# Kernel tuning notes

Measured on AMD Instinct MI355X. Metric: run time of the kernel, lower is better.

## Reference

```python
import jax, jax.numpy as jnp
import numpy as np

B, S, H, R, F, E, K = 4, 2048, 1024, 256, 4096, 8, 2


def setup_inputs() -> dict:
    key = jax.random.key(0)
    k = jax.random.split(key, 7)
    s = 0.02
    return {
        "x": jax.random.normal(k[0], (B, S, H), dtype=jnp.float32),
        "router_w": jax.random.normal(k[1], (H, E), dtype=jnp.float32) * s,
        "router_b": jnp.zeros((E,), dtype=jnp.float32),
        "w1": jax.random.normal(k[2], (E, H, R), dtype=jnp.float32) * s,  # expert Linear(hidden->rank), no bias
        "w2": jax.random.normal(k[3], (E, R, F), dtype=jnp.float32) * s,  # expert Linear(rank->ffn), no bias
        "lin2_w": jax.random.normal(k[4], (F, H), dtype=jnp.float32) * s,
        "lin2_b": jnp.zeros((H,), dtype=jnp.float32),
    }


def reference(x, router_w, router_b, w1, w2, lin2_w, lin2_b):
    # Router: softmax over experts, top-k selection (mask), weight by softmax prob
    logits = jnp.einsum("bsh,he->bse", x, router_w) + router_b
    routing_weights = jax.nn.softmax(logits, axis=-1)            # [B,S,E]
    _, topk_idx = jax.lax.top_k(routing_weights, K)              # [B,S,K]
    mask = jnp.sum(jax.nn.one_hot(topk_idx, E, dtype=x.dtype), axis=-2)  # [B,S,E] in {0,1}
    mw = routing_weights * mask                                  # mask * weight per expert

    # Dense per-expert low-rank FFN (original computes all experts, masks after).
    # Fold mask*weight into the rank-space activations to avoid a [B,S,E,F] tensor.
    t = jnp.einsum("bsh,ehr->bser", x, w1)                       # [B,S,E,R]
    t = t * mw[..., None]
    mixed = jnp.einsum("bser,erf->bsf", t, w2)                   # [B,S,F]

    h = jax.nn.gelu(mixed, approximate=False)                    # torch nn.GELU is erf-based
    out = jnp.einsum("bsf,fh->bsh", h, lin2_w) + lin2_b
    # dropout is identity in eval mode
    return out
```

## Files before the change

### kernel.cpp

```cpp
#include <hip/hip_runtime.h>
#include <math.h>


using short8  = __attribute__((ext_vector_type(8))) short;
using floatx4 = __attribute__((ext_vector_type(4))) float;
typedef unsigned short bf16_t;

#define TOK   8192
#define HDIM  1024
#define RDIM  256
#define FDIM  4096
#define NEXP  8
#define MAXTILES 128
#define MAXSLOTS 16384

__device__ __forceinline__ bf16_t f2bf(float f) {
  union { float f; unsigned u; } a; a.f = f;
  unsigned u = a.u;
  return (bf16_t)((u + 0x7FFFu + ((u >> 16) & 1u)) >> 16);
}

__device__ __forceinline__ float gelu_erf(float v) {
  return 0.5f * v * (1.0f + erff(v * 0.70710678118654752f));
}

__device__ __forceinline__ void gload16(const void* g, void* l) {
  __builtin_amdgcn_global_load_lds(
      (const __attribute__((address_space(1))) void*)g,
      (__attribute__((address_space(3))) void*)l, 16, 0, 0);
}


__global__ void tcvt(const float* __restrict__ in, bf16_t* __restrict__ out,
                     int cols, size_t inSlice, size_t ldo,
                     int outRowStep, int outColStep) {
  __shared__ float tile[32][33];
  const int z  = blockIdx.z;
  const float* src = in + (size_t)z * inSlice;
  const int c0 = blockIdx.x * 32;
  const int r0 = blockIdx.y * 32;
  const int tx = threadIdx.x;
  const int ty = threadIdx.y;
#pragma unroll
  for (int i = 0; i < 32; i += 8)
    tile[ty + i][tx] = src[(size_t)(r0 + ty + i) * cols + (c0 + tx)];
  __syncthreads();
#pragma unroll
  for (int i = 0; i < 32; i += 8) {
    float v = tile[tx][ty + i];
    out[((size_t)(c0 + ty + i) + (size_t)z * outRowStep) * ldo +
        (size_t)z * outColStep + (r0 + tx)] = f2bf(v);
  }
}


__global__ void zero_ctrl(int* ctrl) {
  ctrl[blockIdx.x * 256 + threadIdx.x] = 0;
}

__global__ void router_kernel(const float* __restrict__ x,
                              const float* __restrict__ rw,
                              const float* __restrict__ rb,
                              int* __restrict__ ctrl,
                              int* __restrict__ gid_tok,
                              float2* __restrict__ tokscale,
                              bf16_t* __restrict__ xb) {
  const int token = blockIdx.x * 4 + (threadIdx.x >> 6);
  const int lane  = threadIdx.x & 63;
  const float* xr = x + (size_t)token * HDIM;
  bf16_t* xbr = xb + (size_t)token * HDIM;

  double acc[NEXP];
#pragma unroll
  for (int e = 0; e < NEXP; e++) acc[e] = 0.0;
  for (int h = lane; h < HDIM; h += 64) {
    const float xf = xr[h];
    xbr[h] = f2bf(xf);
    const double xv = (double)xf;
    const float* wr = rw + (size_t)h * NEXP;
#pragma unroll
    for (int e = 0; e < NEXP; e++) acc[e] += xv * (double)wr[e];
  }
#pragma unroll
  for (int off = 32; off > 0; off >>= 1) {
#pragma unroll
    for (int e = 0; e < NEXP; e++) acc[e] += __shfl_xor(acc[e], off, 64);
  }
  double lg[NEXP];
#pragma unroll
  for (int e = 0; e < NEXP; e++) lg[e] = acc[e] + (double)rb[e];

  double mx = lg[0];
#pragma unroll
  for (int e = 1; e < NEXP; e++) mx = fmax(mx, lg[e]);
  double p[NEXP]; double den = 0.0;
#pragma unroll
  for (int e = 0; e < NEXP; e++) { p[e] = exp(lg[e] - mx); den += p[e]; }

  int i1 = 0;
#pragma unroll
  for (int e = 1; e < NEXP; e++) if (lg[e] > lg[i1]) i1 = e;
  int i2 = (i1 == 0) ? 1 : 0;
#pragma unroll
  for (int e = 0; e < NEXP; e++)
    if (e != i1 && e != i2 && lg[e] > lg[i2]) i2 = e;

  if (lane == 0) {
    const int elo = min(i1, i2), ehi = max(i1, i2);
    const int gid = elo * 8 + ehi;
    gid_tok[token] = gid;
    tokscale[token] = make_float2((float)(p[elo] / den), (float)(p[ehi] / den));
    atomicAdd(&ctrl[gid], 1);
  }
}

__global__ void build_tiles(int* __restrict__ ctrl, int* __restrict__ tok_of_slot,
                            float2* __restrict__ scale_of_slot) {
  __shared__ int cnt[64], ntl[64];
  const int t = threadIdx.x;
  for (int i = t; i < MAXSLOTS; i += 256) {
    tok_of_slot[i] = -1;
    scale_of_slot[i] = make_float2(0.f, 0.f);
  }
  if (t < 64) {
    const int c = ctrl[t];
    cnt[t] = c;
    ntl[t] = (c + 127) >> 7;
    ctrl[64 + t] = 0;
  }
  __syncthreads();
  if (t < 64) {
    int slot0 = 0, tile0 = 0;
    for (int g = 0; g < t; g++) { slot0 += ntl[g] << 7; tile0 += ntl[g]; }
    ctrl[128 + t] = slot0;
    const int nt = ntl[t], c = cnt[t];
    for (int i = 0; i < nt; i++) {
      ctrl[256 + (tile0 + i) * 3 + 0] = t;
      ctrl[256 + (tile0 + i) * 3 + 1] = slot0 + i * 128;
      ctrl[256 + (tile0 + i) * 3 + 2] = min(128, c - i * 128);
    }
    if (t == 63) ctrl[192] = tile0 + nt;
  }
}

__global__ void scatter_tokens(const int* __restrict__ gid_tok,
                               const float2* __restrict__ tokscale,
                               int* __restrict__ ctrl,
                               int* __restrict__ tok_of_slot,
                               float2* __restrict__ scale_of_slot) {
  const int t = blockIdx.x * 256 + threadIdx.x;
  const int g = gid_tok[t];
  const int pos = atomicAdd(&ctrl[64 + g], 1);
  const int slot = ctrl[128 + g] + pos;
  tok_of_slot[slot] = t;
  scale_of_slot[slot] = tokscale[t];
}


__global__ __launch_bounds__(256)
void gemm_g1(const bf16_t* __restrict__ xb, const bf16_t* __restrict__ w1t,
             bf16_t* __restrict__ Tp, const int* __restrict__ ctrl,
             const int* __restrict__ tok_of_slot,
             const float2* __restrict__ scale_of_slot) {
  const int b = blockIdx.x;
  const int tile = b >> 3, nt = b & 7;
  if (tile >= ctrl[192]) return;
  __shared__ bf16_t As[128 * 64];
  __shared__ bf16_t Bs[64 * 64];
  const int gid   = ctrl[256 + tile * 3];
  const int slot0 = ctrl[256 + tile * 3 + 1];
  const int e = (nt < 4) ? (gid >> 3) : (gid & 7);
  const int tid = threadIdx.x, lane = tid & 63, w = tid >> 6;
  const int l16 = lane & 15, quad = lane >> 4;
  const int rl = lane >> 3, gg = lane & 7;
  const int gf = (gg ^ rl) * 8;

  floatx4 acc[2][4];
  const floatx4 zero = {0.f, 0.f, 0.f, 0.f};
#pragma unroll
  for (int i = 0; i < 2; i++)
#pragma unroll
    for (int j = 0; j < 4; j++) acc[i][j] = zero;

  const bf16_t* ga[4];
#pragma unroll
  for (int c = 0; c < 4; c++) {
    int tk = tok_of_slot[slot0 + w * 32 + c * 8 + rl];
    if (tk < 0) tk = 0;
    ga[c] = xb + (size_t)tk * HDIM + gf;
  }
  const bf16_t* gb[2];
#pragma unroll
  for (int c = 0; c < 2; c++)
    gb[c] = w1t + (size_t)(e * 256 + (nt & 3) * 64 + w * 16 + c * 8 + rl) * HDIM + gf;
  bf16_t* lA = &As[w * 32 * 64];
  bf16_t* lB = &Bs[w * 16 * 64];

  for (int k0 = 0; k0 < HDIM; k0 += 64) {
    __syncthreads();
#pragma unroll
    for (int c = 0; c < 4; c++) { gload16(ga[c], lA + c * 512); ga[c] += 64; }
#pragma unroll
    for (int c = 0; c < 2; c++) { gload16(gb[c], lB + c * 512); gb[c] += 64; }
    __syncthreads();
#pragma unroll
    for (int s = 0; s < 2; s++) {
      const int pg = ((s * 4 + quad) ^ (l16 & 7)) * 8;
      short8 af[2], bfr[4];
#pragma unroll
      for (int i = 0; i < 2; i++)
        af[i] = *(const short8*)&As[(w * 32 + i * 16 + l16) * 64 + pg];
#pragma unroll
      for (int i = 0; i < 4; i++)
        bfr[i] = *(const short8*)&Bs[(i * 16 + l16) * 64 + pg];
#pragma unroll
      for (int mi = 0; mi < 2; mi++)
#pragma unroll
        for (int ni = 0; ni < 4; ni++)
          acc[mi][ni] = __builtin_amdgcn_mfma_f32_16x16x32_bf16(
              af[mi], bfr[ni], acc[mi][ni], 0, 0, 0);
    }
  }

#pragma unroll
  for (int mi = 0; mi < 2; mi++) {
#pragma unroll
    for (int r = 0; r < 4; r++) {
      const int srow = slot0 + w * 32 + mi * 16 + quad * 4 + r;
      const float2 sc = scale_of_slot[srow];
      const float s = (nt < 4) ? sc.x : sc.y;
#pragma unroll
      for (int ni = 0; ni < 4; ni++) {
        const int col = nt * 64 + ni * 16 + l16;
        Tp[(size_t)srow * 512 + col] = f2bf(acc[mi][ni][r] * s);
      }
    }
  }
}

__global__ __launch_bounds__(256)
void gemm_g2(const bf16_t* __restrict__ Tp, const bf16_t* __restrict__ w2t,
             bf16_t* __restrict__ Hb, const int* __restrict__ ctrl,
             const int* __restrict__ tok_of_slot) {
  const int b = blockIdx.x;
  const int tile = b >> 5, n = b & 31;
  if (tile >= ctrl[192]) return;
  __shared__ bf16_t As[128 * 64];
  __shared__ bf16_t Bs[128 * 64];
  const int gid   = ctrl[256 + tile * 3];
  const int slot0 = ctrl[256 + tile * 3 + 1];
  const int n0 = n * 128;
  const int elo = gid >> 3, ehi = gid & 7;
  const int tid = threadIdx.x, lane = tid & 63, w = tid >> 6;
  const int wm = (w >> 1) * 64, wn = (w & 1) * 64;
  const int l16 = lane & 15, quad = lane >> 4;
  const int rl = lane >> 3, gg = lane & 7;
  const int gf = (gg ^ rl) * 8;

  floatx4 acc[4][4];
  const floatx4 zero = {0.f, 0.f, 0.f, 0.f};
#pragma unroll
  for (int i = 0; i < 4; i++)
#pragma unroll
    for (int j = 0; j < 4; j++) acc[i][j] = zero;

  const bf16_t* ga[4];
  const bf16_t* gbr[4];
#pragma unroll
  for (int c = 0; c < 4; c++) {
    ga[c]  = Tp + (size_t)(slot0 + w * 32 + c * 8 + rl) * 512 + gf;
    gbr[c] = w2t + (size_t)(n0 + w * 32 + c * 8 + rl) * 2048 + gf;
  }
  bf16_t* lA = &As[w * 32 * 64];
  bf16_t* lB = &Bs[w * 32 * 64];

#pragma unroll
  for (int t = 0; t < 8; t++) {
    const int e = (t < 4) ? elo : ehi;
    const int bcol = e * 256 + (t & 3) * 64;
    __syncthreads();
#pragma unroll
    for (int c = 0; c < 4; c++) { gload16(ga[c], lA + c * 512); ga[c] += 64; }
#pragma unroll
    for (int c = 0; c < 4; c++) gload16(gbr[c] + bcol, lB + c * 512);
    __syncthreads();
#pragma unroll
    for (int s = 0; s < 2; s++) {
      const int pg = ((s * 4 + quad) ^ (l16 & 7)) * 8;
      short8 af[4], bfr[4];
#pragma unroll
      for (int i = 0; i < 4; i++)
        af[i] = *(const short8*)&As[(wm + i * 16 + l16) * 64 + pg];
#pragma unroll
      for (int i = 0; i < 4; i++)
        bfr[i] = *(const short8*)&Bs[(wn + i * 16 + l16) * 64 + pg];
#pragma unroll
      for (int mi = 0; mi < 4; mi++)
#pragma unroll
        for (int ni = 0; ni < 4; ni++)
          acc[mi][ni] = __builtin_amdgcn_mfma_f32_16x16x32_bf16(
              af[mi], bfr[ni], acc[mi][ni], 0, 0, 0);
    }
  }

#pragma unroll
  for (int mi = 0; mi < 4; mi++) {
#pragma unroll
    for (int r = 0; r < 4; r++) {
      const int srow = slot0 + wm + mi * 16 + quad * 4 + r;
      const int tok = tok_of_slot[srow];
      if (tok < 0) continue;
#pragma unroll
      for (int ni = 0; ni < 4; ni++) {
        const int col = n0 + wn + ni * 16 + l16;
        Hb[(size_t)tok * FDIM + col] = f2bf(gelu_erf(acc[mi][ni][r]));
      }
    }
  }
}

__global__ __launch_bounds__(256)
void gemm_g3(const bf16_t* __restrict__ Hb, const bf16_t* __restrict__ ltw,
             float* __restrict__ out, const float* __restrict__ bias) {
  __shared__ bf16_t As[128 * 64];
  __shared__ bf16_t Bs[64 * 64];
  const int b = blockIdx.x;
  const int xcd = b & 7, j = b >> 3;
  const int m0 = (xcd * 8 + (j & 7)) * 128;
  const int n0 = (j >> 3) * 64;
  const int tid = threadIdx.x, lane = tid & 63, w = tid >> 6;
  const int l16 = lane & 15, quad = lane >> 4;
  const int rl = lane >> 3, gg = lane & 7;
  const int gf = (gg ^ rl) * 8;

  floatx4 acc[2][4];
  const floatx4 zero = {0.f, 0.f, 0.f, 0.f};
#pragma unroll
  for (int i = 0; i < 2; i++)
#pragma unroll
    for (int j2 = 0; j2 < 4; j2++) acc[i][j2] = zero;

  const bf16_t* ga[4];
#pragma unroll
  for (int c = 0; c < 4; c++)
    ga[c] = Hb + (size_t)(m0 + w * 32 + c * 8 + rl) * FDIM + gf;
  const bf16_t* gb[2];
#pragma unroll
  for (int c = 0; c < 2; c++)
    gb[c] = ltw + (size_t)(n0 + w * 16 + c * 8 + rl) * FDIM + gf;
  bf16_t* lA = &As[w * 32 * 64];
  bf16_t* lB = &Bs[w * 16 * 64];

  for (int k0 = 0; k0 < FDIM; k0 += 64) {
    __syncthreads();
#pragma unroll
    for (int c = 0; c < 4; c++) { gload16(ga[c], lA + c * 512); ga[c] += 64; }
#pragma unroll
    for (int c = 0; c < 2; c++) { gload16(gb[c], lB + c * 512); gb[c] += 64; }
    __syncthreads();
#pragma unroll
    for (int s = 0; s < 2; s++) {
      const int pg = ((s * 4 + quad) ^ (l16 & 7)) * 8;
      short8 af[2], bfr[4];
#pragma unroll
      for (int i = 0; i < 2; i++)
        af[i] = *(const short8*)&As[(w * 32 + i * 16 + l16) * 64 + pg];
#pragma unroll
      for (int i = 0; i < 4; i++)
        bfr[i] = *(const short8*)&Bs[(i * 16 + l16) * 64 + pg];
#pragma unroll
      for (int mi = 0; mi < 2; mi++)
#pragma unroll
        for (int ni = 0; ni < 4; ni++)
          acc[mi][ni] = __builtin_amdgcn_mfma_f32_16x16x32_bf16(
              af[mi], bfr[ni], acc[mi][ni], 0, 0, 0);
    }
  }

#pragma unroll
  for (int mi = 0; mi < 2; mi++) {
#pragma unroll
    for (int ni = 0; ni < 4; ni++) {
      const int row = m0 + w * 32 + mi * 16 + quad * 4;
      const int col = n0 + ni * 16 + l16;
#pragma unroll
      for (int r = 0; r < 4; r++)
        out[(size_t)(row + r) * HDIM + col] = acc[mi][ni][r] + bias[col];
    }
  }
}


extern "C" void kernel_launch(void* const* d_in, const int* in_sizes, int n_in,
                              void* d_out, int out_size, void* d_ws, size_t ws_size,
                              hipStream_t stream) {
  const float* x   = (const float*)d_in[0];
  const float* rw  = (const float*)d_in[1];
  const float* rb  = (const float*)d_in[2];
  const float* w1  = (const float*)d_in[3];
  const float* w2  = (const float*)d_in[4];
  const float* l2w = (const float*)d_in[5];
  const float* l2b = (const float*)d_in[6];

  char* ws = (char*)d_ws;
  int*    ctrl     = (int*)   (ws + 0);
  int*    gid_tok  = (int*)   (ws + 4096);
  float2* tokscale = (float2*)(ws + 36864);
  int*    tokslot  = (int*)   (ws + 102400);
  float2* slotsc   = (float2*)(ws + 167936);
  bf16_t* xb  = (bf16_t*)(ws + 1048576);
  bf16_t* w1t = (bf16_t*)(ws + 17825792);
  bf16_t* w2t = (bf16_t*)(ws + 22020096);
  bf16_t* ltw = (bf16_t*)(ws + 38797312);
  bf16_t* Tp  = (bf16_t*)(ws + 47185920);
  bf16_t* Hb  = (bf16_t*)(ws + 63963136);

  zero_ctrl<<<4, 256, 0, stream>>>(ctrl);
  router_kernel<<<TOK / 4, 256, 0, stream>>>(x, rw, rb, ctrl, gid_tok, tokscale, xb);
  build_tiles<<<1, 256, 0, stream>>>(ctrl, tokslot, slotsc);
  scatter_tokens<<<TOK / 256, 256, 0, stream>>>(gid_tok, tokscale, ctrl, tokslot, slotsc);

  tcvt<<<dim3(RDIM / 32, HDIM / 32, NEXP), dim3(32, 8), 0, stream>>>(
      w1, w1t, RDIM, (size_t)HDIM * RDIM, HDIM, RDIM, 0);
  tcvt<<<dim3(FDIM / 32, RDIM / 32, NEXP), dim3(32, 8), 0, stream>>>(
      w2, w2t, FDIM, (size_t)RDIM * FDIM, 2048, 0, RDIM);
  tcvt<<<dim3(HDIM / 32, FDIM / 32, 1), dim3(32, 8), 0, stream>>>(
      l2w, ltw, HDIM, 0, FDIM, 0, 0);

  gemm_g1<<<8 * MAXTILES, 256, 0, stream>>>(xb, w1t, Tp, ctrl, tokslot, slotsc);
  gemm_g2<<<32 * MAXTILES, 256, 0, stream>>>(Tp, w2t, Hb, ctrl, tokslot);
  gemm_g3<<<(TOK / 128) * (HDIM / 64), 256, 0, stream>>>(Hb, ltw, (float*)d_out, l2b);
}
```

Before: 397.7 us.

## Enlarge final GEMM tile, move histogram into build_tiles, retile transposes and grid order

The final output GEMM now uses 128x128 tiles with a 2x2 warp layout, which halves the block count and raises reuse of each loaded A tile. The expert-pair histogram moves from global atomics in the router into shared-memory atomics inside the single-block build_tiles kernel, so the zero_ctrl launch goes away. The weight transposes use 64x64 tiles. The MoE GEMM grids are reordered so that the tile index varies fastest, and MAXTILES drops to 96. The risks are that the serial histogram in one block adds latency, and that a cap of 96 tiles could overflow if the routing is very uneven.

```diff
diff --git a/kernel.cpp b/kernel.cpp
--- a/kernel.cpp
+++ b/kernel.cpp
@@ -11,7 +11,7 @@
 #define RDIM  256
 #define FDIM  4096
 #define NEXP  8
-#define MAXTILES 128
+#define MAXTILES 96
 #define MAXSLOTS 16384
 
 __device__ __forceinline__ bf16_t f2bf(float f) {
@@ -34,19 +34,19 @@
 __global__ void tcvt(const float* __restrict__ in, bf16_t* __restrict__ out,
                      int cols, size_t inSlice, size_t ldo,
                      int outRowStep, int outColStep) {
-  __shared__ float tile[32][33];
+  __shared__ float tile[64][65];
   const int z  = blockIdx.z;
   const float* src = in + (size_t)z * inSlice;
-  const int c0 = blockIdx.x * 32;
-  const int r0 = blockIdx.y * 32;
+  const int c0 = blockIdx.x * 64;
+  const int r0 = blockIdx.y * 64;
   const int tx = threadIdx.x;
   const int ty = threadIdx.y;
 #pragma unroll
-  for (int i = 0; i < 32; i += 8)
+  for (int i = 0; i < 64; i += 4)
     tile[ty + i][tx] = src[(size_t)(r0 + ty + i) * cols + (c0 + tx)];
   __syncthreads();
 #pragma unroll
-  for (int i = 0; i < 32; i += 8) {
+  for (int i = 0; i < 64; i += 4) {
     float v = tile[tx][ty + i];
     out[((size_t)(c0 + ty + i) + (size_t)z * outRowStep) * ldo +
         (size_t)z * outColStep + (r0 + tx)] = f2bf(v);
@@ -54,14 +54,9 @@
 }
 
 
-__global__ void zero_ctrl(int* ctrl) {
-  ctrl[blockIdx.x * 256 + threadIdx.x] = 0;
-}
-
 __global__ void router_kernel(const float* __restrict__ x,
                               const float* __restrict__ rw,
                               const float* __restrict__ rb,
-                              int* __restrict__ ctrl,
                               int* __restrict__ gid_tok,
                               float2* __restrict__ tokscale,
                               bf16_t* __restrict__ xb) {
@@ -107,33 +102,33 @@
 
   if (lane == 0) {
     const int elo = min(i1, i2), ehi = max(i1, i2);
-    const int gid = elo * 8 + ehi;
-    gid_tok[token] = gid;
+    gid_tok[token] = elo * 8 + ehi;
     tokscale[token] = make_float2((float)(p[elo] / den), (float)(p[ehi] / den));
-    atomicAdd(&ctrl[gid], 1);
-  }
-}
-
-__global__ void build_tiles(int* __restrict__ ctrl, int* __restrict__ tok_of_slot,
+  }
+}
+
+__global__ void build_tiles(const int* __restrict__ gid_tok,
+                            int* __restrict__ ctrl,
+                            int* __restrict__ tok_of_slot,
                             float2* __restrict__ scale_of_slot) {
-  __shared__ int cnt[64], ntl[64];
+  __shared__ int hist[64], ntl[64];
   const int t = threadIdx.x;
   for (int i = t; i < MAXSLOTS; i += 256) {
     tok_of_slot[i] = -1;
     scale_of_slot[i] = make_float2(0.f, 0.f);
   }
-  if (t < 64) {
-    const int c = ctrl[t];
-    cnt[t] = c;
-    ntl[t] = (c + 127) >> 7;
-    ctrl[64 + t] = 0;
-  }
+  if (t < 64) { hist[t] = 0; }
+  __syncthreads();
+  for (int i = t; i < TOK; i += 256) atomicAdd(&hist[gid_tok[i]], 1);
+  __syncthreads();
+  if (t < 64) ntl[t] = (hist[t] + 127) >> 7;
   __syncthreads();
   if (t < 64) {
     int slot0 = 0, tile0 = 0;
     for (int g = 0; g < t; g++) { slot0 += ntl[g] << 7; tile0 += ntl[g]; }
+    ctrl[64 + t] = 0;
     ctrl[128 + t] = slot0;
-    const int nt = ntl[t], c = cnt[t];
+    const int nt = ntl[t], c = hist[t];
     for (int i = 0; i < nt; i++) {
       ctrl[256 + (tile0 + i) * 3 + 0] = t;
       ctrl[256 + (tile0 + i) * 3 + 1] = slot0 + i * 128;
@@ -163,7 +158,7 @@
              const int* __restrict__ tok_of_slot,
              const float2* __restrict__ scale_of_slot) {
   const int b = blockIdx.x;
-  const int tile = b >> 3, nt = b & 7;
+  const int tile = b % MAXTILES, nt = b / MAXTILES;
   if (tile >= ctrl[192]) return;
   __shared__ bf16_t As[128 * 64];
   __shared__ bf16_t Bs[64 * 64];
@@ -243,7 +238,7 @@
              bf16_t* __restrict__ Hb, const int* __restrict__ ctrl,
              const int* __restrict__ tok_of_slot) {
   const int b = blockIdx.x;
-  const int tile = b >> 5, n = b & 31;
+  const int tile = b % MAXTILES, n = b / MAXTILES;
   if (tile >= ctrl[192]) return;
   __shared__ bf16_t As[128 * 64];
   __shared__ bf16_t Bs[128 * 64];
@@ -323,53 +318,52 @@
 void gemm_g3(const bf16_t* __restrict__ Hb, const bf16_t* __restrict__ ltw,
              float* __restrict__ out, const float* __restrict__ bias) {
   __shared__ bf16_t As[128 * 64];
-  __shared__ bf16_t Bs[64 * 64];
+  __shared__ bf16_t Bs[128 * 64];
   const int b = blockIdx.x;
-  const int xcd = b & 7, j = b >> 3;
-  const int m0 = (xcd * 8 + (j & 7)) * 128;
-  const int n0 = (j >> 3) * 64;
+  const int m0 = ((b & 7) * 8 + ((b >> 3) & 7)) * 128;
+  const int n0 = (b >> 6) * 128;
   const int tid = threadIdx.x, lane = tid & 63, w = tid >> 6;
+  const int wm = (w >> 1) * 64, wn = (w & 1) * 64;
   const int l16 = lane & 15, quad = lane >> 4;
   const int rl = lane >> 3, gg = lane & 7;
   const int gf = (gg ^ rl) * 8;
 
-  floatx4 acc[2][4];
+  floatx4 acc[4][4];
   const floatx4 zero = {0.f, 0.f, 0.f, 0.f};
 #pragma unroll
-  for (int i = 0; i < 2; i++)
-#pragma unroll
-    for (int j2 = 0; j2 < 4; j2++) acc[i][j2] = zero;
+  for (int i = 0; i < 4; i++)
+#pragma unroll
+    for (int j = 0; j < 4; j++) acc[i][j] = zero;
 
   const bf16_t* ga[4];
-#pragma unroll
-  for (int c = 0; c < 4; c++)
-    ga[c] = Hb + (size_t)(m0 + w * 32 + c * 8 + rl) * FDIM + gf;
-  const bf16_t* gb[2];
-#pragma unroll
-  for (int c = 0; c < 2; c++)
-    gb[c] = ltw + (size_t)(n0 + w * 16 + c * 8 + rl) * FDIM + gf;
+  const bf16_t* gb[4];
+#pragma unroll
+  for (int c = 0; c < 4; c++) {
+    ga[c] = Hb  + (size_t)(m0 + w * 32 + c * 8 + rl) * FDIM + gf;
+    gb[c] = ltw + (size_t)(n0 + w * 32 + c * 8 + rl) * FDIM + gf;
+  }
   bf16_t* lA = &As[w * 32 * 64];
-  bf16_t* lB = &Bs[w * 16 * 64];
+  bf16_t* lB = &Bs[w * 32 * 64];
 
   for (int k0 = 0; k0 < FDIM; k0 += 64) {
     __syncthreads();
 #pragma unroll
     for (int c = 0; c < 4; c++) { gload16(ga[c], lA + c * 512); ga[c] += 64; }
 #pragma unroll
-    for (int c = 0; c < 2; c++) { gload16(gb[c], lB + c * 512); gb[c] += 64; }
+    for (int c = 0; c < 4; c++) { gload16(gb[c], lB + c * 512); gb[c] += 64; }
     __syncthreads();
 #pragma unroll
     for (int s = 0; s < 2; s++) {
       const int pg = ((s * 4 + quad) ^ (l16 & 7)) * 8;
-      short8 af[2], bfr[4];
-#pragma unroll
-      for (int i = 0; i < 2; i++)
-        af[i] = *(const short8*)&As[(w * 32 + i * 16 + l16) * 64 + pg];
+      short8 af[4], bfr[4];
 #pragma unroll
       for (int i = 0; i < 4; i++)
-        bfr[i] = *(const short8*)&Bs[(i * 16 + l16) * 64 + pg];
-#pragma unroll
-      for (int mi = 0; mi < 2; mi++)
+        af[i] = *(const short8*)&As[(wm + i * 16 + l16) * 64 + pg];
+#pragma unroll
+      for (int i = 0; i < 4; i++)
+        bfr[i] = *(const short8*)&Bs[(wn + i * 16 + l16) * 64 + pg];
+#pragma unroll
+      for (int mi = 0; mi < 4; mi++)
 #pragma unroll
         for (int ni = 0; ni < 4; ni++)
           acc[mi][ni] = __builtin_amdgcn_mfma_f32_16x16x32_bf16(
@@ -378,11 +372,11 @@
   }
 
 #pragma unroll
-  for (int mi = 0; mi < 2; mi++) {
+  for (int mi = 0; mi < 4; mi++) {
 #pragma unroll
     for (int ni = 0; ni < 4; ni++) {
-      const int row = m0 + w * 32 + mi * 16 + quad * 4;
-      const int col = n0 + ni * 16 + l16;
+      const int row = m0 + wm + mi * 16 + quad * 4;
+      const int col = n0 + wn + ni * 16 + l16;
 #pragma unroll
       for (int r = 0; r < 4; r++)
         out[(size_t)(row + r) * HDIM + col] = acc[mi][ni][r] + bias[col];
@@ -415,19 +409,18 @@
   bf16_t* Tp  = (bf16_t*)(ws + 47185920);
   bf16_t* Hb  = (bf16_t*)(ws + 63963136);
 
-  zero_ctrl<<<4, 256, 0, stream>>>(ctrl);
-  router_kernel<<<TOK / 4, 256, 0, stream>>>(x, rw, rb, ctrl, gid_tok, tokscale, xb);
-  build_tiles<<<1, 256, 0, stream>>>(ctrl, tokslot, slotsc);
+  router_kernel<<<TOK / 4, 256, 0, stream>>>(x, rw, rb, gid_tok, tokscale, xb);
+  build_tiles<<<1, 256, 0, stream>>>(gid_tok, ctrl, tokslot, slotsc);
   scatter_tokens<<<TOK / 256, 256, 0, stream>>>(gid_tok, tokscale, ctrl, tokslot, slotsc);
 
-  tcvt<<<dim3(RDIM / 32, HDIM / 32, NEXP), dim3(32, 8), 0, stream>>>(
+  tcvt<<<dim3(RDIM / 64, HDIM / 64, NEXP), dim3(64, 4), 0, stream>>>(
       w1, w1t, RDIM, (size_t)HDIM * RDIM, HDIM, RDIM, 0);
-  tcvt<<<dim3(FDIM / 32, RDIM / 32, NEXP), dim3(32, 8), 0, stream>>>(
+  tcvt<<<dim3(FDIM / 64, RDIM / 64, NEXP), dim3(64, 4), 0, stream>>>(
       w2, w2t, FDIM, (size_t)RDIM * FDIM, 2048, 0, RDIM);
-  tcvt<<<dim3(HDIM / 32, FDIM / 32, 1), dim3(32, 8), 0, stream>>>(
+  tcvt<<<dim3(HDIM / 64, FDIM / 64, 1), dim3(64, 4), 0, stream>>>(
       l2w, ltw, HDIM, 0, FDIM, 0, 0);
 
   gemm_g1<<<8 * MAXTILES, 256, 0, stream>>>(xb, w1t, Tp, ctrl, tokslot, slotsc);
   gemm_g2<<<32 * MAXTILES, 256, 0, stream>>>(Tp, w2t, Hb, ctrl, tokslot);
-  gemm_g3<<<(TOK / 128) * (HDIM / 64), 256, 0, stream>>>(Hb, ltw, (float*)d_out, l2b);
-}
+  gemm_g3<<<512, 256, 0, stream>>>(Hb, ltw, (float*)d_out, l2b);
+}
```

Result: faster. 366.2 us (-7.9%).
